# Optimization experiments

Measured on AMD Instinct MI355X. Metric: run time of the kernel, lower is better.

The kernel has to match this reference:

```python
import jax, jax.numpy as jnp
import numpy as np
from functools import partial

TAU = 2.0
BN_EPS = 1e-5
SG_ALPHA = 4.0  # spikingjelly surrogate.Sigmoid default

@jax.custom_vjp
def heaviside(x):
    return (x >= 0.0).astype(x.dtype)

def _heaviside_fwd(x):
    return heaviside(x), x

def _heaviside_bwd(x, g):
    s = jax.nn.sigmoid(SG_ALPHA * x)
    return (g * SG_ALPHA * s * (1.0 - s),)

heaviside.defvjp(_heaviside_fwd, _heaviside_bwd)

def lif(x_seq, v_threshold=1.0):
    # MultiStepLIFNode: tau=2, decay_input=True, v_reset=0 (hard reset), detach_reset
    def step(v, x):
        v = v + (x - v) / TAU
        s = heaviside(v - v_threshold)
        v = v * (1.0 - jax.lax.stop_gradient(s))
        return v, s
    _, s_seq = jax.lax.scan(step, jnp.zeros_like(x_seq[0]), x_seq)
    return s_seq

def conv1x1_bn(x, w, gamma, beta, mean, var, b=None):
    # x: [T,B,C,N]; w: [Cout,Cin]; 1x1 conv == channel matmul; BN in eval mode
    y = jnp.einsum('oc,tbcn->tbon', w, x)
    if b is not None:
        y = y + b[:, None]
    inv = gamma / jnp.sqrt(var + BN_EPS)
    return y * inv[:, None] + (beta - mean * inv)[:, None]

def setup_inputs() -> dict:
    key = jax.random.key(0)
    ks = jax.random.split(key, 24)
    T, B, C, N = 4, 32, 384, 196
    d = {}
    d['x'] = jax.random.normal(ks[0], (T, B, C, N), dtype=jnp.float32)
    d['policy'] = jax.random.uniform(ks[1], (T * B, N, 1), dtype=jnp.float32)
    scale = 1.0 / np.sqrt(C)
    for i, p in enumerate(['q', 'k', 'v', 'proj']):
        base = 2 + i * 5
        d[p + '_w'] = jax.random.normal(ks[base], (C, C), dtype=jnp.float32) * scale
        d[p + '_gamma'] = jnp.ones((C,), jnp.float32)
        d[p + '_beta'] = jnp.zeros((C,), jnp.float32)
        d[p + '_mean'] = jax.random.normal(ks[base + 1], (C,), dtype=jnp.float32) * 0.1
        d[p + '_var'] = jax.random.uniform(ks[base + 2], (C,), dtype=jnp.float32, minval=0.5, maxval=1.5)
    d['proj_b'] = jnp.zeros((C,), jnp.float32)
    return d

def _to_heads(s, H):
    T, B, C, N = s.shape
    # [T,B,C,N] -> [T,B,N,H,D] -> [T,B,H,N,D]
    return s.transpose(0, 1, 3, 2).reshape(T, B, N, H, C // H).transpose(0, 1, 3, 2, 4)

def reference(x, policy, q_w, q_gamma, q_beta, q_mean, q_var,
              k_w, k_gamma, k_beta, k_mean, k_var,
              v_w, v_gamma, v_beta, v_mean, v_var,
              proj_w, proj_gamma, proj_beta, proj_mean, proj_var, proj_b):
    T, B, C, N = x.shape
    H = 12
    attn_scale = 0.25
    q = _to_heads(lif(conv1x1_bn(x, q_w, q_gamma, q_beta, q_mean, q_var)), H)
    k = _to_heads(lif(conv1x1_bn(x, k_w, k_gamma, k_beta, k_mean, k_var)), H)
    v = _to_heads(lif(conv1x1_bn(x, v_w, v_gamma, v_beta, v_mean, v_var)), H)
    attn = jnp.einsum('tbhnd,tbhmd->tbhnm', q, k)
    # attention_policy: attn *= (policy + (1-policy)*eye)
    pol = policy.reshape(T, B, 1, 1, N)
    eye = jnp.eye(N, dtype=attn.dtype)
    attn = attn * (pol + (1.0 - pol) * eye)
    y = jnp.einsum('tbhnm,tbhmd->tbhnd', attn, v) * attn_scale
    y = y.transpose(0, 1, 2, 4, 3).reshape(T, B, C, N)
    y = lif(y, v_threshold=0.5)
    y = conv1x1_bn(y, proj_w, proj_gamma, proj_beta, proj_mean, proj_var, b=proj_b)
    return lif(y)
```

## Files before the change

### kernel.cpp

```cpp
#include <hip/hip_runtime.h>

typedef unsigned int u32;
typedef __bf16 bf16x8 __attribute__((ext_vector_type(8)));
typedef __bf16 bf16x4v __attribute__((ext_vector_type(4)));
typedef _Float16 f16x8 __attribute__((ext_vector_type(8)));
typedef float f32x4 __attribute__((ext_vector_type(4)));

#define Tn 4
#define Bn 32
#define Cn 384
#define Nn 196
#define Hn 12
#define CNn (Cn*Nn)
#define BCNn (Bn*CNn)
#define BHNn (Bn*Hn*Nn)
#define PBITS (Tn*BHNn)
#define TBCNn (Tn*BCNn)
#define NCOLS 6272
#define WSZ 147456

__device__ __forceinline__ void split3(float v, __bf16& h, __bf16& m, __bf16& l) {
  h = (__bf16)v;  float r = v - (float)h;
  m = (__bf16)r;  float r2 = r - (float)m;
  l = (__bf16)r2;
}
__device__ __forceinline__ void split2h(float v, _Float16& h, _Float16& l) {
  h = (_Float16)v;  l = (_Float16)(v - (float)h);
}

__device__ __forceinline__ void gl_lds16(const void* g, void* l) {
  __builtin_amdgcn_global_load_lds(
      (const __attribute__((address_space(1))) unsigned int*)g,
      (__attribute__((address_space(3))) unsigned int*)l, 16, 0, 0);
}

struct WSplitArgs {
  const float* w[4]; const float* g[4]; const float* be[4];
  const float* mu[4]; const float* va[4]; const float* bias;
};
__global__ __launch_bounds__(256) void prep(
    WSplitArgs a, _Float16* __restrict__ wsp16, __bf16* __restrict__ wspb,
    float* __restrict__ shv, const float* __restrict__ x,
    _Float16* __restrict__ xs) {
  __shared__ float tile[49 * 130];
  const int bx = blockIdx.x;
  const int tid = threadIdx.x;
  if (bx < 2304) {
    const int i = bx * 256 + tid;
    const int p = i / WSZ, r = i - p * WSZ;
    const int o = r / Cn;
    const float iv = a.g[p][o] / sqrtf(a.va[p][o] + 1e-5f);
    const float wv = a.w[p][r] * iv;
    if (p < 3) {
      _Float16 h, l;
      split2h(wv, h, l);
      wsp16[(size_t)(p * 2 + 0) * WSZ + r] = h;
      wsp16[(size_t)(p * 2 + 1) * WSZ + r] = l;
    } else {
      __bf16 h, m, l;
      split3(wv, h, m, l);
      wspb[(size_t)0 * WSZ + r] = h;
      wspb[(size_t)1 * WSZ + r] = m;
      wspb[(size_t)2 * WSZ + r] = l;
    }
    if (r - o * Cn == 0) {
      float sh = a.be[p][o] - a.mu[p][o] * iv;
      if (p == 3) sh += a.bias[o] * iv;
      shv[p * Cn + o] = sh;
    }
    return;
  }
  const int bid2 = bx - 2304;
  const int t = bid2 & 3, b = (bid2 >> 2) & 31, zz = bid2 >> 7;
  const int ct = zz >> 2, nch = zz & 3;
  const int c0 = ct * 128, n0 = nch * 49;
  for (int idx = tid; idx < 49 * 128; idx += 256) {
    const int n = idx % 49, c = idx / 49;
    tile[n * 130 + c] = x[(size_t)t * BCNn + (size_t)b * CNn +
                          (size_t)(c0 + c) * Nn + n0 + n];
  }
  __syncthreads();
  for (int idx = tid; idx < 49 * 64; idx += 256) {
    const int cp = idx & 63, n = idx >> 6;
    const float v0 = tile[n * 130 + cp * 2];
    const float v1 = tile[n * 130 + cp * 2 + 1];
    _Float16 h0, l0, h1, l1;
    split2h(v0, h0, l0);
    split2h(v1, h1, l1);
    const size_t col = (size_t)t * NCOLS + (size_t)b * Nn + n0 + n;
    union { _Float16 f[2]; u32 u; } uh, ul;
    uh.f[0] = h0; uh.f[1] = h1;
    ul.f[0] = l0; ul.f[1] = l1;
    ((u32*)(xs + col * Cn + c0))[cp] = uh.u;
    ((u32*)(xs + (size_t)TBCNn + col * Cn + c0))[cp] = ul.u;
  }
}

__global__ __launch_bounds__(256, 2) void gemm_qkv_lif(
    const _Float16* __restrict__ xs,
    const _Float16* __restrict__ wsp16,
    const float* __restrict__ shv,
    u32* __restrict__ bq, u32* __restrict__ bk, u32* __restrict__ bv)
{
  __shared__ _Float16 Asw[3][2][128][32];
  __shared__ _Float16 Bsw[3][2][64][32];
  const int orig = blockIdx.x;
  const int xcd = orig & 7, i8 = orig >> 3;
  const int wgid = xcd * 110 + (xcd < 2 ? xcd : 2) + i8;
  const int colt = wgid / 9, v = wgid - colt * 9;
  const int col0 = colt * 64;
  const int p = v / 3, mt = v - p * 3;
  const int o0 = mt * 128;
  const int tid = threadIdx.x, lane = tid & 63, wid = tid >> 6;
  const int wm = wid >> 1, wn = wid & 1;
  const int quad = lane >> 4, nl = lane & 15;
  u32* __restrict__ bits = (p == 0) ? bq : (p == 1) ? bk : bv;

  u32 aOff[4], bOff[2];
#pragma unroll
  for (int i = 0; i < 4; ++i) {
    const int c = i * 256 + wid * 64 + lane;
    const int s = c >> 9, row = (c >> 2) & 127, kb = c & 3;
    const int kbs = kb ^ ((row >> 1) & 3);
    aOff[i] = (u32)((((p * 2 + s) * WSZ) + (o0 + row) * Cn + kbs * 8) * 2);
  }
#pragma unroll
  for (int i = 0; i < 2; ++i) {
    const int c = i * 256 + wid * 64 + lane;
    const int s = c >> 8, rem = c & 255, row = rem >> 2, kb = rem & 3;
    const int kbs = kb ^ ((row >> 1) & 3);
    bOff[i] = (u32)(((size_t)s * TBCNn + (size_t)(col0 + row) * Cn + kbs * 8) * 2);
  }
  const char* wB = (const char*)wsp16;
  const char* xB = (const char*)xs;
  char* aD0 = (char*)&Asw[0][0][0][0] + wid * 1024;
  char* bD0 = (char*)&Bsw[0][0][0][0] + wid * 1024;

#define STAGE_A(ai_) do {                                                  \
    const u32 ak_ = (u32)(((ai_) % 12) * 64);                              \
    char* d_ = aD0 + ((ai_) % 3) * 16384;                                  \
    _Pragma("unroll") for (int i_ = 0; i_ < 4; ++i_)                       \
      gl_lds16(wB + aOff[i_] + ak_, d_ + i_ * 4096);                       \
  } while (0)
#define STAGE_B(g_) do {                                                   \
    const int t_ = ((g_) / 24) * 2 + ((g_) & 1);                           \
    const int kk_ = (((g_) % 24) >> 1);                                    \
    const u32 bk_ = (u32)(kk_ * 64) + (u32)t_ * (u32)(NCOLS * Cn * 2);     \
    char* d_ = bD0 + ((g_) % 3) * 8192;                                    \
    _Pragma("unroll") for (int i_ = 0; i_ < 2; ++i_)                       \
      gl_lds16(xB + bOff[i_] + bk_, d_ + i_ * 4096);                       \
  } while (0)

  f32x4 sh_[4];
#pragma unroll
  for (int mi = 0; mi < 4; ++mi)
    sh_[mi] = *(const f32x4*)&shv[p * Cn + o0 + wm * 64 + mi * 16 + quad * 4];

  f32x4 acc0[4][2], acc1[4][2];
  f32x4 vst[4][2] = {};

  auto epi = [&](f32x4 (&ac)[4][2], int t) {
#pragma unroll
    for (int ni = 0; ni < 2; ++ni) {
      u32 w0 = 0, w1 = 0;
#pragma unroll
      for (int mi = 0; mi < 4; ++mi) {
#pragma unroll
        for (int r = 0; r < 4; ++r) {
          const float y = ac[mi][ni][r] + sh_[mi][r];
          const float vv = vst[mi][ni][r];
          const float nv = vv + (y - vv) * 0.5f;
          const bool sk = nv >= 1.0f;
          vst[mi][ni][r] = sk ? 0.f : nv;
          const u32 b1 = sk ? 1u : 0u;
          const int pos = ((mi & 1) << 4) + (quad << 2) + r;
          if (mi < 2) w0 |= b1 << pos; else w1 |= b1 << pos;
        }
      }
      w0 |= __shfl_xor(w0, 16); w0 |= __shfl_xor(w0, 32);
      w1 |= __shfl_xor(w1, 16); w1 |= __shfl_xor(w1, 32);
      if (quad == 0) {
        const int col = col0 + wn * 32 + ni * 16 + nl;
        const int bb = col / Nn, nn = col - bb * Nn;
        u32* bp = bits + (size_t)t * BHNn +
                  ((size_t)bb * Hn + (mt * 4 + wm * 2)) * Nn + nn;
        bp[0] = w0;
        bp[Nn] = w1;
      }
    }
  };

  STAGE_B(0); STAGE_A(0); STAGE_B(1); STAGE_A(1);

#pragma unroll 1
  for (int gg = 0; gg < 24; ++gg) {
    const int abuf = gg % 3;
    const int be = (2 * gg) % 3, bo = (2 * gg + 1) % 3;
    const int kk = gg % 12;

    if (gg < 23) { asm volatile("s_waitcnt vmcnt(6)" ::: "memory"); }
    else         { asm volatile("s_waitcnt vmcnt(2)" ::: "memory"); }
    __builtin_amdgcn_s_barrier();
    __builtin_amdgcn_sched_barrier(0);
    if (gg < 23) STAGE_B(2 * gg + 2);
    if (kk == 0) {
#pragma unroll
      for (int mi = 0; mi < 4; ++mi)
#pragma unroll
        for (int ni = 0; ni < 2; ++ni) {
          acc0[mi][ni] = f32x4{0.f, 0.f, 0.f, 0.f};
          acc1[mi][ni] = f32x4{0.f, 0.f, 0.f, 0.f};
        }
    }
    f16x8 af0[4], af1[4];
#pragma unroll
    for (int mi = 0; mi < 4; ++mi) {
      const int ra = wm * 64 + mi * 16 + nl;
      const int ka = (quad ^ ((ra >> 1) & 3)) * 8;
      af0[mi] = *(const f16x8*)&Asw[abuf][0][ra][ka];
      af1[mi] = *(const f16x8*)&Asw[abuf][1][ra][ka];
    }
    {
      f16x8 bfr[2][2];
#pragma unroll
      for (int i = 0; i < 2; ++i) {
        const int rb = wn * 32 + i * 16 + nl;
        const int kb2 = (quad ^ ((rb >> 1) & 3)) * 8;
        bfr[0][i] = *(const f16x8*)&Bsw[be][0][rb][kb2];
        bfr[1][i] = *(const f16x8*)&Bsw[be][1][rb][kb2];
      }
      __builtin_amdgcn_s_setprio(1);
#pragma unroll
      for (int mi = 0; mi < 4; ++mi)
#pragma unroll
        for (int ni = 0; ni < 2; ++ni) {
          f32x4 c = acc0[mi][ni];
          c = __builtin_amdgcn_mfma_f32_16x16x32_f16(af0[mi], bfr[0][ni], c, 0, 0, 0);
          c = __builtin_amdgcn_mfma_f32_16x16x32_f16(af0[mi], bfr[1][ni], c, 0, 0, 0);
          c = __builtin_amdgcn_mfma_f32_16x16x32_f16(af1[mi], bfr[0][ni], c, 0, 0, 0);
          acc0[mi][ni] = c;
        }
      __builtin_amdgcn_s_setprio(0);
    }

    if (gg < 23) { asm volatile("s_waitcnt vmcnt(6)" ::: "memory"); }
    else         { asm volatile("s_waitcnt vmcnt(0)" ::: "memory"); }
    __builtin_amdgcn_s_barrier();
    __builtin_amdgcn_sched_barrier(0);
    if (gg < 23) STAGE_B(2 * gg + 3);
    if (gg < 22) STAGE_A(gg + 2);
    {
      f16x8 bfr[2][2];
#pragma unroll
      for (int i = 0; i < 2; ++i) {
        const int rb = wn * 32 + i * 16 + nl;
        const int kb2 = (quad ^ ((rb >> 1) & 3)) * 8;
        bfr[0][i] = *(const f16x8*)&Bsw[bo][0][rb][kb2];
        bfr[1][i] = *(const f16x8*)&Bsw[bo][1][rb][kb2];
      }
      __builtin_amdgcn_s_setprio(1);
#pragma unroll
      for (int mi = 0; mi < 4; ++mi)
#pragma unroll
        for (int ni = 0; ni < 2; ++ni) {
          f32x4 c = acc1[mi][ni];
          c = __builtin_amdgcn_mfma_f32_16x16x32_f16(af0[mi], bfr[0][ni], c, 0, 0, 0);
          c = __builtin_amdgcn_mfma_f32_16x16x32_f16(af0[mi], bfr[1][ni], c, 0, 0, 0);
          c = __builtin_amdgcn_mfma_f32_16x16x32_f16(af1[mi], bfr[0][ni], c, 0, 0, 0);
          acc1[mi][ni] = c;
        }
      __builtin_amdgcn_s_setprio(0);
    }
    if (kk == 11) {
      const int p2 = gg / 12;
      epi(acc0, p2 * 2 + 0);
      epi(acc1, p2 * 2 + 1);
    }
  }
#undef STAGE_A
#undef STAGE_B
}

#define ASTR 40
__global__ __launch_bounds__(256) void attn_lif(
    const u32* __restrict__ qb, const u32* __restrict__ kb,
    const u32* __restrict__ vb, const float* __restrict__ policy,
    __bf16* __restrict__ sp) {
  __shared__ u32 qs[208], ks[224], vs_[224];
  __shared__ float ps[224];
  __shared__ __bf16 psp[3][224];
  __shared__ __bf16 Al[112 * ASTR];
  __shared__ __bf16 Ul[3][32 * ASTR];
  const int blk = blockIdx.x;
  const int half = blk & 1;
  const int bh = blk >> 1;
  const int bN = bh / Hn;
  const int h = bh - bN * Hn;
  const int nbase = half * 112;
  const int ntiles = half ? 6 : 7;
  const int nrows = ntiles * 16;
  const int tid = threadIdx.x;
  const int lane = tid & 63, wid = tid >> 6;
  const int quad = lane >> 4, nl = lane & 15;

  float vst[2][2][4] = {};

  for (int t = 0; t < Tn; ++t) {
    const int tb = t * Bn + bN;
    const int gid = tb * Hn + h;
    if (t) __syncthreads();
    for (int i = tid; i < 224; i += 256) {
      const bool in = i < Nn;
      if (i < 208) qs[i] = in ? qb[(size_t)gid * Nn + i] : 0u;
      ks[i] = in ? kb[(size_t)gid * Nn + i] : 0u;
      vs_[i] = in ? vb[(size_t)gid * Nn + i] : 0u;
      const float p = in ? policy[(size_t)tb * Nn + i] : 0.f;
      ps[i] = p;
      __bf16 hh, mm, ll;
      split3(p, hh, mm, ll);
      psp[0][i] = hh; psp[1][i] = mm; psp[2][i] = ll;
    }
    __syncthreads();

    f32x4 acc[2][2] = {};

    for (int slab = 0; slab < 7; ++slab) {
      const int m0 = slab * 32;
      if (tid < nrows) {
        const u32 qn = qs[nbase + tid];
        __bf16 a32[32];
#pragma unroll
        for (int mk = 0; mk < 32; ++mk)
          a32[mk] = (__bf16)(float)__popc(qn & ks[m0 + mk]);
#pragma unroll
        for (int g = 0; g < 4; ++g)
          *(bf16x8*)&Al[tid * ASTR + g * 8] = *(bf16x8*)&a32[g * 8];
      }
      {
        const int dp = tid >> 3, mkg = (tid & 7) * 4;
        __bf16 u4[3][4];
#pragma unroll
        for (int j = 0; j < 4; ++j) {
          const int m = m0 + mkg + j;
          const bool bit = (vs_[m] >> dp) & 1u;
#pragma unroll
          for (int s = 0; s < 3; ++s)
            u4[s][j] = bit ? psp[s][m] : (__bf16)0.f;
        }
#pragma unroll
        for (int s = 0; s < 3; ++s)
          *(bf16x4v*)&Ul[s][dp * ASTR + mkg] = *(bf16x4v*)u4[s];
      }
      __syncthreads();
      bf16x8 bfr[3][2];
#pragma unroll
      for (int s = 0; s < 3; ++s)
#pragma unroll
        for (int nt = 0; nt < 2; ++nt)
          bfr[s][nt] = *(const bf16x8*)&Ul[s][(nt * 16 + nl) * ASTR + quad * 8];
#pragma unroll
      for (int mi = 0; mi < 2; ++mi) {
        const int lt = wid + mi * 4;
        if (lt < ntiles) {
          const bf16x8 af = *(const bf16x8*)&Al[(lt * 16 + nl) * ASTR + quad * 8];
#pragma unroll
          for (int nt = 0; nt < 2; ++nt) {
            f32x4 c = acc[mi][nt];
            c = __builtin_amdgcn_mfma_f32_16x16x32_bf16(af, bfr[0][nt], c, 0, 0, 0);
            c = __builtin_amdgcn_mfma_f32_16x16x32_bf16(af, bfr[1][nt], c, 0, 0, 0);
            c = __builtin_amdgcn_mfma_f32_16x16x32_bf16(af, bfr[2][nt], c, 0, 0, 0);
            acc[mi][nt] = c;
          }
        }
      }
      __syncthreads();
    }
#pragma unroll
    for (int mi = 0; mi < 2; ++mi) {
      const int lt = wid + mi * 4;
      if (lt >= ntiles) continue;
#pragma unroll
      for (int r = 0; r < 4; ++r) {
        const int n = nbase + lt * 16 + quad * 4 + r;
        if (n >= Nn) continue;
        const float ann = (float)__popc(qs[n] & ks[n]);
        const float wd = ann * (1.0f - ps[n]);
        const u32 vn = vs_[n];
        __bf16* op = sp + (size_t)t * BCNn + ((size_t)bN * Nn + n) * Cn + h * 32;
#pragma unroll
        for (int nt = 0; nt < 2; ++nt) {
          const int d = nt * 16 + nl;
          const float bit = (float)((vn >> d) & 1u);
          const float y = (acc[mi][nt][r] + wd * bit) * 0.25f;
          const float vv = vst[mi][nt][r];
          const float nv = vv + (y - vv) * 0.5f;
          const bool s = nv >= 0.5f;
          vst[mi][nt][r] = s ? 0.f : nv;
          op[d] = (__bf16)(s ? 1.0f : 0.0f);
        }
      }
    }
  }
}

__global__ __launch_bounds__(256, 3) void gemm_proj_mfma(
    const __bf16* __restrict__ sp, const __bf16* __restrict__ wspb,
    const float* __restrict__ shv, float* __restrict__ z)
{
  __shared__ __bf16 Asw[3][128][32];
  __shared__ __bf16 Bsw[128][32];
  const int bid = blockIdx.x;
  const int xcd = bid & 7, slot = bid >> 3;
  const int gl = slot / 3, mt = slot - gl * 3;
  const int group = xcd * 25 + gl;
  if (group >= 196) return;
  const int colt = group % 49, t = group / 49;
  const int col0 = colt * 128, o0 = mt * 128;
  const int tid = threadIdx.x, lane = tid & 63, wid = tid >> 6;
  const int wm = wid >> 1, wn = wid & 1;
  const int quad = lane >> 4, nl = lane & 15;
  const __bf16* Bg = sp + ((size_t)t * NCOLS + col0) * Cn;

  const char* aSrc[6];
  const char* bSrc[2];
#pragma unroll
  for (int i = 0; i < 6; ++i) {
    const int c = i * 256 + wid * 64 + lane;
    const int s = c >> 9, rem = c & 511;
    const int row = rem >> 2, kb = rem & 3;
    const int kbs = kb ^ ((row >> 1) & 3);
    aSrc[i] = (const char*)(wspb + (size_t)s * WSZ +
                            (size_t)(o0 + row) * Cn + kbs * 8);
  }
#pragma unroll
  for (int i = 0; i < 2; ++i) {
    const int c = i * 256 + wid * 64 + lane;
    const int row = c >> 2, kb = c & 3;
    const int kbs = kb ^ ((row >> 1) & 3);
    bSrc[i] = (const char*)(Bg + (size_t)row * Cn + kbs * 8);
  }
  char* aDst = (char*)&Asw[0][0][0] + wid * 1024;
  char* bDst = (char*)&Bsw[0][0] + wid * 1024;

  f32x4 acc[4][4] = {};

  for (int kk = 0; kk < 12; ++kk) {
    const int koff = kk * 64;
#pragma unroll
    for (int i = 0; i < 6; ++i) gl_lds16(aSrc[i] + koff, aDst + i * 4096);
#pragma unroll
    for (int i = 0; i < 2; ++i) gl_lds16(bSrc[i] + koff, bDst + i * 4096);
    __syncthreads();
    bf16x8 af[3][4], bfr[4];
#pragma unroll
    for (int i = 0; i < 4; ++i) {
      const int ra = wm * 64 + i * 16 + nl;
      const int rb = wn * 64 + i * 16 + nl;
      const int ka = (quad ^ ((ra >> 1) & 3)) * 8;
      const int kb2 = (quad ^ ((rb >> 1) & 3)) * 8;
      bfr[i] = *(const bf16x8*)&Bsw[rb][kb2];
#pragma unroll
      for (int s = 0; s < 3; ++s)
        af[s][i] = *(const bf16x8*)&Asw[s][ra][ka];
    }
#pragma unroll
    for (int mi = 0; mi < 4; ++mi)
#pragma unroll
      for (int ni = 0; ni < 4; ++ni) {
        f32x4 c = acc[mi][ni];
        c = __builtin_amdgcn_mfma_f32_16x16x32_bf16(af[0][mi], bfr[ni], c, 0, 0, 0);
        c = __builtin_amdgcn_mfma_f32_16x16x32_bf16(af[1][mi], bfr[ni], c, 0, 0, 0);
        c = __builtin_amdgcn_mfma_f32_16x16x32_bf16(af[2][mi], bfr[ni], c, 0, 0, 0);
        acc[mi][ni] = c;
      }
    __syncthreads();
  }
#pragma unroll
  for (int mi = 0; mi < 4; ++mi) {
    const int ob = o0 + wm * 64 + mi * 16 + quad * 4;
    const f32x4 sh4 = *(const f32x4*)&shv[3 * Cn + ob];
#pragma unroll
    for (int ni = 0; ni < 4; ++ni) {
      const int col = col0 + wn * 64 + ni * 16 + nl;
      const int b = col / Nn, nn = col - b * Nn;
      float* zp = z + (size_t)t * BCNn + (size_t)b * CNn + nn;
#pragma unroll
      for (int r = 0; r < 4; ++r)
        zp[(size_t)(ob + r) * Nn] = acc[mi][ni][r] + sh4[r];
    }
  }
}

__global__ __launch_bounds__(256) void lif_out_v4(
    const float* __restrict__ z, float* __restrict__ out) {
  const size_t i4 = ((size_t)blockIdx.x * 256 + threadIdx.x) * 4;
  f32x4 v = {0.f, 0.f, 0.f, 0.f};
#pragma unroll
  for (int t = 0; t < Tn; ++t) {
    f32x4 x = *(const f32x4*)(z + (size_t)t * BCNn + i4);
    f32x4 o4;
#pragma unroll
    for (int r = 0; r < 4; ++r) {
      const float nv = v[r] + (x[r] - v[r]) * 0.5f;
      const bool s = nv >= 1.0f;
      o4[r] = s ? 1.0f : 0.0f;
      v[r] = s ? 0.f : nv;
    }
    *(f32x4*)(out + (size_t)t * BCNn + i4) = o4;
  }
}

extern "C" void kernel_launch(void* const* d_in, const int* in_sizes, int n_in,
                              void* d_out, int out_size, void* d_ws, size_t ws_size,
                              hipStream_t stream) {
  const float* x      = (const float*)d_in[0];
  const float* policy = (const float*)d_in[1];
  const float* qw = (const float*)d_in[2];
  const float* qg = (const float*)d_in[3];
  const float* qb_ = (const float*)d_in[4];
  const float* qm = (const float*)d_in[5];
  const float* qv = (const float*)d_in[6];
  const float* kw = (const float*)d_in[7];
  const float* kg = (const float*)d_in[8];
  const float* kbe = (const float*)d_in[9];
  const float* km = (const float*)d_in[10];
  const float* kv = (const float*)d_in[11];
  const float* vw = (const float*)d_in[12];
  const float* vg = (const float*)d_in[13];
  const float* vbe = (const float*)d_in[14];
  const float* vm = (const float*)d_in[15];
  const float* vv = (const float*)d_in[16];
  const float* pw = (const float*)d_in[17];
  const float* pg = (const float*)d_in[18];
  const float* pbe = (const float*)d_in[19];
  const float* pm = (const float*)d_in[20];
  const float* pv = (const float*)d_in[21];
  const float* pbias = (const float*)d_in[22];
  float* out = (float*)d_out;

  char* base = (char*)d_ws;
  _Float16* xs   = (_Float16*)base;
  _Float16* wsp16 = (_Float16*)(base + (size_t)TBCNn * 4);
  __bf16* wspb   = (__bf16*)((char*)wsp16 + (size_t)6 * WSZ * 2);
  float* shv     = (float*)((char*)wspb + (size_t)3 * WSZ * 2);
  u32* bq        = (u32*)((char*)shv + 4 * Cn * 4);
  u32* bk = bq + PBITS;
  u32* bv = bk + PBITS;
  __bf16* sp     = (__bf16*)(bv + PBITS);
  float* z       = (float*)((char*)sp + (size_t)TBCNn * 2);

  WSplitArgs wa;
  wa.w[0] = qw; wa.g[0] = qg; wa.be[0] = qb_; wa.mu[0] = qm; wa.va[0] = qv;
  wa.w[1] = kw; wa.g[1] = kg; wa.be[1] = kbe; wa.mu[1] = km; wa.va[1] = kv;
  wa.w[2] = vw; wa.g[2] = vg; wa.be[2] = vbe; wa.mu[2] = vm; wa.va[2] = vv;
  wa.w[3] = pw; wa.g[3] = pg; wa.be[3] = pbe; wa.mu[3] = pm; wa.va[3] = pv;
  wa.bias = pbias;
  prep<<<3840, 256, 0, stream>>>(wa, wsp16, wspb, shv, x, xs);

  gemm_qkv_lif<<<882, 256, 0, stream>>>(xs, wsp16, shv, bq, bk, bv);
  attn_lif<<<2 * Bn * Hn, 256, 0, stream>>>(bq, bk, bv, policy, sp);
  gemm_proj_mfma<<<600, 256, 0, stream>>>(sp, wspb, shv, z);
  lif_out_v4<<<BCNn / 1024, 256, 0, stream>>>(z, out);
}
```

Baseline: 296.9 us.

## Fuse output LIF into projection GEMM with pipelined time-step loop

The projection GEMM now loops over all four time steps inside each block, using 64x64 tiles. It keeps the LIF membrane state in registers and writes spikes directly, which removes the separate lif_out kernel and the float z intermediate round-trip. Loads use triple-buffered LDS with explicit vmcnt waits and barriers, and two time steps are processed per weight tile so the A fragments are reused. The attention kernel also splits popcount row generation across two threads per row. Tiles are smaller and each block's work is serialized across time, so there is less parallelism per block.

```diff
diff --git a/kernel.cpp b/kernel.cpp
--- a/kernel.cpp
+++ b/kernel.cpp
@@ -302,6 +302,7 @@
   const int tid = threadIdx.x;
   const int lane = tid & 63, wid = tid >> 6;
   const int quad = lane >> 4, nl = lane & 15;
+  const int arow = tid >> 1, ag = (tid & 1) << 4;
 
   float vst[2][2][4] = {};
 
@@ -326,15 +327,14 @@
 
     for (int slab = 0; slab < 7; ++slab) {
       const int m0 = slab * 32;
-      if (tid < nrows) {
-        const u32 qn = qs[nbase + tid];
-        __bf16 a32[32];
-#pragma unroll
-        for (int mk = 0; mk < 32; ++mk)
-          a32[mk] = (__bf16)(float)__popc(qn & ks[m0 + mk]);
-#pragma unroll
-        for (int g = 0; g < 4; ++g)
-          *(bf16x8*)&Al[tid * ASTR + g * 8] = *(bf16x8*)&a32[g * 8];
+      if (arow < nrows) {
+        const u32 qn = qs[nbase + arow];
+        __bf16 a16[16];
+#pragma unroll
+        for (int mk = 0; mk < 16; ++mk)
+          a16[mk] = (__bf16)(float)__popc(qn & ks[m0 + ag + mk]);
+        *(bf16x8*)&Al[arow * ASTR + ag] = *(bf16x8*)&a16[0];
+        *(bf16x8*)&Al[arow * ASTR + ag + 8] = *(bf16x8*)&a16[8];
       }
       {
         const int dp = tid >> 3, mkg = (tid & 7) * 4;
@@ -403,111 +403,172 @@
   }
 }
 
-__global__ __launch_bounds__(256, 3) void gemm_proj_mfma(
+__global__ __launch_bounds__(256, 3) void gemm_proj_lif(
     const __bf16* __restrict__ sp, const __bf16* __restrict__ wspb,
-    const float* __restrict__ shv, float* __restrict__ z)
+    const float* __restrict__ shv, float* __restrict__ out)
 {
-  __shared__ __bf16 Asw[3][128][32];
-  __shared__ __bf16 Bsw[128][32];
-  const int bid = blockIdx.x;
-  const int xcd = bid & 7, slot = bid >> 3;
-  const int gl = slot / 3, mt = slot - gl * 3;
-  const int group = xcd * 25 + gl;
-  if (group >= 196) return;
-  const int colt = group % 49, t = group / 49;
-  const int col0 = colt * 128, o0 = mt * 128;
+  __shared__ __bf16 Asw[3][3][64][32];
+  __shared__ __bf16 Bsw[3][64][32];
+  const int orig = blockIdx.x;
+  const int xcd = orig & 7, i8 = orig >> 3;
+  const int wgid = xcd * 73 + (xcd < 4 ? xcd : 4) + i8;
+  const int colt = wgid / 6, ot = wgid - colt * 6;
+  const int col0 = colt * 64;
+  const int o0 = ot * 64;
   const int tid = threadIdx.x, lane = tid & 63, wid = tid >> 6;
   const int wm = wid >> 1, wn = wid & 1;
   const int quad = lane >> 4, nl = lane & 15;
-  const __bf16* Bg = sp + ((size_t)t * NCOLS + col0) * Cn;
-
-  const char* aSrc[6];
-  const char* bSrc[2];
-#pragma unroll
-  for (int i = 0; i < 6; ++i) {
+
+  u32 aOff[3], bOff;
+#pragma unroll
+  for (int i = 0; i < 3; ++i) {
     const int c = i * 256 + wid * 64 + lane;
-    const int s = c >> 9, rem = c & 511;
-    const int row = rem >> 2, kb = rem & 3;
+    const int s = c >> 8, rem = c & 255, row = rem >> 2, kb = rem & 3;
     const int kbs = kb ^ ((row >> 1) & 3);
-    aSrc[i] = (const char*)(wspb + (size_t)s * WSZ +
-                            (size_t)(o0 + row) * Cn + kbs * 8);
-  }
-#pragma unroll
-  for (int i = 0; i < 2; ++i) {
-    const int c = i * 256 + wid * 64 + lane;
+    aOff[i] = (u32)(((s * WSZ) + (o0 + row) * Cn + kbs * 8) * 2);
+  }
+  {
+    const int c = wid * 64 + lane;
     const int row = c >> 2, kb = c & 3;
     const int kbs = kb ^ ((row >> 1) & 3);
-    bSrc[i] = (const char*)(Bg + (size_t)row * Cn + kbs * 8);
-  }
-  char* aDst = (char*)&Asw[0][0][0] + wid * 1024;
-  char* bDst = (char*)&Bsw[0][0] + wid * 1024;
-
-  f32x4 acc[4][4] = {};
-
-  for (int kk = 0; kk < 12; ++kk) {
-    const int koff = kk * 64;
-#pragma unroll
-    for (int i = 0; i < 6; ++i) gl_lds16(aSrc[i] + koff, aDst + i * 4096);
-#pragma unroll
-    for (int i = 0; i < 2; ++i) gl_lds16(bSrc[i] + koff, bDst + i * 4096);
-    __syncthreads();
-    bf16x8 af[3][4], bfr[4];
-#pragma unroll
-    for (int i = 0; i < 4; ++i) {
-      const int ra = wm * 64 + i * 16 + nl;
-      const int rb = wn * 64 + i * 16 + nl;
+    bOff = (u32)(((size_t)(col0 + row) * Cn + kbs * 8) * 2);
+  }
+  const char* wB = (const char*)wspb;
+  const char* sB = (const char*)sp;
+  char* aD0 = (char*)&Asw[0][0][0][0] + wid * 1024;
+  char* bD0 = (char*)&Bsw[0][0][0] + wid * 1024;
+
+#define STAGE_A(ai_) do {                                                  \
+    const u32 ak_ = (u32)(((ai_) % 12) * 64);                              \
+    char* d_ = aD0 + ((ai_) % 3) * 12288;                                  \
+    _Pragma("unroll") for (int i_ = 0; i_ < 3; ++i_)                       \
+      gl_lds16(wB + aOff[i_] + ak_, d_ + i_ * 4096);                       \
+  } while (0)
+#define STAGE_B(g_) do {                                                   \
+    const int t_ = ((g_) / 24) * 2 + ((g_) & 1);                           \
+    const int kk_ = (((g_) % 24) >> 1);                                    \
+    const u32 bk_ = (u32)(kk_ * 64) + (u32)t_ * (u32)(BCNn * 2);           \
+    gl_lds16(sB + bOff + bk_, bD0 + ((g_) % 3) * 4096);                    \
+  } while (0)
+
+  f32x4 sh_[2];
+#pragma unroll
+  for (int mi = 0; mi < 2; ++mi)
+    sh_[mi] = *(const f32x4*)&shv[3 * Cn + o0 + wm * 32 + mi * 16 + quad * 4];
+
+  f32x4 acc0[2][2], acc1[2][2];
+  f32x4 vst[2][2] = {};
+
+  auto epi = [&](f32x4 (&ac)[2][2], int t) {
+#pragma unroll
+    for (int mi = 0; mi < 2; ++mi) {
+      const int ob = o0 + wm * 32 + mi * 16 + quad * 4;
+#pragma unroll
+      for (int ni = 0; ni < 2; ++ni) {
+        const int col = col0 + wn * 32 + ni * 16 + nl;
+        const int bb = col / Nn, nn = col - bb * Nn;
+        float* op = out + (size_t)t * BCNn + (size_t)bb * CNn + nn;
+#pragma unroll
+        for (int r = 0; r < 4; ++r) {
+          const float y = ac[mi][ni][r] + sh_[mi][r];
+          const float vv = vst[mi][ni][r];
+          const float nv = vv + (y - vv) * 0.5f;
+          const bool sk = nv >= 1.0f;
+          vst[mi][ni][r] = sk ? 0.f : nv;
+          op[(size_t)(ob + r) * Nn] = sk ? 1.0f : 0.0f;
+        }
+      }
+    }
+  };
+
+  STAGE_B(0); STAGE_A(0); STAGE_B(1); STAGE_A(1);
+
+#pragma unroll 1
+  for (int gg = 0; gg < 24; ++gg) {
+    const int abuf = gg % 3;
+    const int be = (2 * gg) % 3, bo = (2 * gg + 1) % 3;
+    const int kk = gg % 12;
+
+    if (gg < 23) { asm volatile("s_waitcnt vmcnt(4)" ::: "memory"); }
+    else         { asm volatile("s_waitcnt vmcnt(1)" ::: "memory"); }
+    __builtin_amdgcn_s_barrier();
+    __builtin_amdgcn_sched_barrier(0);
+    if (gg < 23) STAGE_B(2 * gg + 2);
+    if (kk == 0) {
+#pragma unroll
+      for (int mi = 0; mi < 2; ++mi)
+#pragma unroll
+        for (int ni = 0; ni < 2; ++ni) {
+          acc0[mi][ni] = f32x4{0.f, 0.f, 0.f, 0.f};
+          acc1[mi][ni] = f32x4{0.f, 0.f, 0.f, 0.f};
+        }
+    }
+    bf16x8 af[3][2];
+#pragma unroll
+    for (int mi = 0; mi < 2; ++mi) {
+      const int ra = wm * 32 + mi * 16 + nl;
       const int ka = (quad ^ ((ra >> 1) & 3)) * 8;
-      const int kb2 = (quad ^ ((rb >> 1) & 3)) * 8;
-      bfr[i] = *(const bf16x8*)&Bsw[rb][kb2];
 #pragma unroll
       for (int s = 0; s < 3; ++s)
-        af[s][i] = *(const bf16x8*)&Asw[s][ra][ka];
-    }
-#pragma unroll
-    for (int mi = 0; mi < 4; ++mi)
-#pragma unroll
-      for (int ni = 0; ni < 4; ++ni) {
-        f32x4 c = acc[mi][ni];
-        c = __builtin_amdgcn_mfma_f32_16x16x32_bf16(af[0][mi], bfr[ni], c, 0, 0, 0);
-        c = __builtin_amdgcn_mfma_f32_16x16x32_bf16(af[1][mi], bfr[ni], c, 0, 0, 0);
-        c = __builtin_amdgcn_mfma_f32_16x16x32_bf16(af[2][mi], bfr[ni], c, 0, 0, 0);
-        acc[mi][ni] = c;
-      }
-    __syncthreads();
-  }
-#pragma unroll
-  for (int mi = 0; mi < 4; ++mi) {
-    const int ob = o0 + wm * 64 + mi * 16 + quad * 4;
-    const f32x4 sh4 = *(const f32x4*)&shv[3 * Cn + ob];
-#pragma unroll
-    for (int ni = 0; ni < 4; ++ni) {
-      const int col = col0 + wn * 64 + ni * 16 + nl;
-      const int b = col / Nn, nn = col - b * Nn;
-      float* zp = z + (size_t)t * BCNn + (size_t)b * CNn + nn;
-#pragma unroll
-      for (int r = 0; r < 4; ++r)
-        zp[(size_t)(ob + r) * Nn] = acc[mi][ni][r] + sh4[r];
-    }
-  }
-}
-
-__global__ __launch_bounds__(256) void lif_out_v4(
-    const float* __restrict__ z, float* __restrict__ out) {
-  const size_t i4 = ((size_t)blockIdx.x * 256 + threadIdx.x) * 4;
-  f32x4 v = {0.f, 0.f, 0.f, 0.f};
-#pragma unroll
-  for (int t = 0; t < Tn; ++t) {
-    f32x4 x = *(const f32x4*)(z + (size_t)t * BCNn + i4);
-    f32x4 o4;
-#pragma unroll
-    for (int r = 0; r < 4; ++r) {
-      const float nv = v[r] + (x[r] - v[r]) * 0.5f;
-      const bool s = nv >= 1.0f;
-      o4[r] = s ? 1.0f : 0.0f;
-      v[r] = s ? 0.f : nv;
-    }
-    *(f32x4*)(out + (size_t)t * BCNn + i4) = o4;
-  }
+        af[s][mi] = *(const bf16x8*)&Asw[abuf][s][ra][ka];
+    }
+    {
+      bf16x8 bfr[2];
+#pragma unroll
+      for (int ni = 0; ni < 2; ++ni) {
+        const int rb = wn * 32 + ni * 16 + nl;
+        const int kb2 = (quad ^ ((rb >> 1) & 3)) * 8;
+        bfr[ni] = *(const bf16x8*)&Bsw[be][rb][kb2];
+      }
+      __builtin_amdgcn_s_setprio(1);
+#pragma unroll
+      for (int mi = 0; mi < 2; ++mi)
+#pragma unroll
+        for (int ni = 0; ni < 2; ++ni) {
+          f32x4 c = acc0[mi][ni];
+          c = __builtin_amdgcn_mfma_f32_16x16x32_bf16(af[0][mi], bfr[ni], c, 0, 0, 0);
+          c = __builtin_amdgcn_mfma_f32_16x16x32_bf16(af[1][mi], bfr[ni], c, 0, 0, 0);
+          c = __builtin_amdgcn_mfma_f32_16x16x32_bf16(af[2][mi], bfr[ni], c, 0, 0, 0);
+          acc0[mi][ni] = c;
+        }
+      __builtin_amdgcn_s_setprio(0);
+    }
+
+    if (gg < 23) { asm volatile("s_waitcnt vmcnt(4)" ::: "memory"); }
+    else         { asm volatile("s_waitcnt vmcnt(0)" ::: "memory"); }
+    __builtin_amdgcn_s_barrier();
+    __builtin_amdgcn_sched_barrier(0);
+    if (gg < 23) STAGE_B(2 * gg + 3);
+    if (gg < 22) STAGE_A(gg + 2);
+    {
+      bf16x8 bfr[2];
+#pragma unroll
+      for (int ni = 0; ni < 2; ++ni) {
+        const int rb = wn * 32 + ni * 16 + nl;
+        const int kb2 = (quad ^ ((rb >> 1) & 3)) * 8;
+        bfr[ni] = *(const bf16x8*)&Bsw[bo][rb][kb2];
+      }
+      __builtin_amdgcn_s_setprio(1);
+#pragma unroll
+      for (int mi = 0; mi < 2; ++mi)
+#pragma unroll
+        for (int ni = 0; ni < 2; ++ni) {
+          f32x4 c = acc1[mi][ni];
+          c = __builtin_amdgcn_mfma_f32_16x16x32_bf16(af[0][mi], bfr[ni], c, 0, 0, 0);
+          c = __builtin_amdgcn_mfma_f32_16x16x32_bf16(af[1][mi], bfr[ni], c, 0, 0, 0);
+          c = __builtin_amdgcn_mfma_f32_16x16x32_bf16(af[2][mi], bfr[ni], c, 0, 0, 0);
+          acc1[mi][ni] = c;
+        }
+      __builtin_amdgcn_s_setprio(0);
+    }
+    if (kk == 11) {
+      const int p2 = gg / 12;
+      epi(acc0, p2 * 2 + 0);
+      epi(acc1, p2 * 2 + 1);
+    }
+  }
+#undef STAGE_A
+#undef STAGE_B
 }
 
 extern "C" void kernel_launch(void* const* d_in, const int* in_sizes, int n_in,
@@ -547,7 +608,6 @@
   u32* bk = bq + PBITS;
   u32* bv = bk + PBITS;
   __bf16* sp     = (__bf16*)(bv + PBITS);
-  float* z       = (float*)((char*)sp + (size_t)TBCNn * 2);
 
   WSplitArgs wa;
   wa.w[0] = qw; wa.g[0] = qg; wa.be[0] = qb_; wa.mu[0] = qm; wa.va[0] = qv;
@@ -559,6 +619,5 @@
 
   gemm_qkv_lif<<<882, 256, 0, stream>>>(xs, wsp16, shv, bq, bk, bv);
   attn_lif<<<2 * Bn * Hn, 256, 0, stream>>>(bq, bk, bv, policy, sp);
-  gemm_proj_mfma<<<600, 256, 0, stream>>>(sp, wspb, shv, z);
-  lif_out_v4<<<BCNn / 1024, 256, 0, stream>>>(z, out);
-}
+  gemm_proj_lif<<<588, 256, 0, stream>>>(sp, wspb, shv, out);
+}
```

Result: no change. 299.6 us (+0.9%).
